# Kernel tuning notes

Hardware: AMD Instinct MI355X
Metric: run time of the kernel (lower is better)

Reference implementation:

```python
import jax, jax.numpy as jnp
import numpy as np

N = 117000   # vocab / number of WordNet synsets (square adjacency)
E = 500000   # number of COO edges
B, T = 4, 64 # batch, seq len


def setup_inputs() -> dict:
    key = jax.random.key(0)
    k1, k2, k3, k4 = jax.random.split(key, 4)
    logits = jax.random.normal(k1, (B, T, N), dtype=jnp.float32)
    # ensure every row index appears at least once so row-normalization never divides by zero
    row = jnp.concatenate([jnp.arange(N, dtype=jnp.int32),
                           jax.random.randint(k2, (E - N,), 0, N, dtype=jnp.int32)])
    col = jax.random.randint(k3, (E,), 0, N, dtype=jnp.int32)
    edge_index = jnp.stack([row, col], axis=0)  # [2, E]
    vv = jax.random.uniform(k4, (E,), dtype=jnp.float32, minval=0.1, maxval=1.0)
    return {"logits": logits, "vv": vv, "edge_index": edge_index}


def reference(logits, vv, edge_index):
    # StructuredLogits.forward with DEHARDCODE_ALPHA=1.0, renormalize=True:
    #   neighbors = spmm(A, logits_flat^T)^T ; neighbors /= row_sum ; out = neighbors + logits
    row, col = edge_index[0], edge_index[1]
    n = logits.shape[-1]
    x = logits.reshape(-1, n).T                              # [N, BT]
    contrib = vv[:, None] * x[col]                           # [E, BT] gather + scale
    neigh_T = jax.ops.segment_sum(contrib, row, num_segments=n)   # [N, BT] scatter-add (SpMM)
    row_sum = jax.ops.segment_sum(vv, row, num_segments=n)        # [N] row-normalizer
    neighbors = (neigh_T / row_sum[:, None]).T.reshape(logits.shape)
    return neighbors + logits
```

## Files before the change

kernel.cpp:

```cpp
#include <hip/hip_runtime.h>
#include <hip/hip_fp16.h>

#define NN 117000
#define BT 256

#define SCAN_CHUNK 1024
#define SCAN_NB ((NN + SCAN_CHUNK - 1) / SCAN_CHUNK)
#define SCAN_P2_T 128

#define ROWS_PB 32
#define LDS_STRIDE (BT + 2)

union U8 { uint2 u; __half2 h[2]; };


__global__ void hist_kernel(const int* __restrict__ row, int* __restrict__ count, int E) {
    int e = blockIdx.x * blockDim.x + threadIdx.x;
    if (e < E) atomicAdd(&count[row[e]], 1);
}

__global__ void scan_phase1(const int* __restrict__ count, int* __restrict__ block_sums) {
    __shared__ int s[256];
    int base = blockIdx.x * SCAN_CHUNK + threadIdx.x * 4;
    int sum = 0;
#pragma unroll
    for (int j = 0; j < 4; ++j) {
        int idx = base + j;
        if (idx < NN) sum += count[idx];
    }
    s[threadIdx.x] = sum;
    __syncthreads();
    for (int off = 128; off > 0; off >>= 1) {
        if (threadIdx.x < off) s[threadIdx.x] += s[threadIdx.x + off];
        __syncthreads();
    }
    if (threadIdx.x == 0) block_sums[blockIdx.x] = s[0];
}

__global__ void scan_phase2(int* __restrict__ block_sums, int* __restrict__ row_ptr) {
    __shared__ int s[SCAN_P2_T];
    int t = threadIdx.x;
    int v = (t < SCAN_NB) ? block_sums[t] : 0;
    s[t] = v;
    __syncthreads();
    for (int off = 1; off < SCAN_P2_T; off <<= 1) {
        int u = (t >= off) ? s[t - off] : 0;
        __syncthreads();
        s[t] += u;
        __syncthreads();
    }
    if (t < SCAN_NB) block_sums[t] = (t == 0) ? 0 : s[t - 1];
    if (t == SCAN_P2_T - 1) row_ptr[NN] = s[SCAN_NB - 1];
}

__global__ void scan_phase3(int* __restrict__ row_ptr, const int* __restrict__ block_offs,
                            int* __restrict__ cursor) {
    __shared__ int s[256];
    int base = blockIdx.x * SCAN_CHUNK + threadIdx.x * 4;
    int v[4];
    int sum = 0;
#pragma unroll
    for (int j = 0; j < 4; ++j) {
        int idx = base + j;
        v[j] = (idx < NN) ? row_ptr[idx] : 0;
        sum += v[j];
    }
    s[threadIdx.x] = sum;
    __syncthreads();
    for (int off = 1; off < 256; off <<= 1) {
        int u = (threadIdx.x >= off) ? s[threadIdx.x - off] : 0;
        __syncthreads();
        s[threadIdx.x] += u;
        __syncthreads();
    }
    int prefix = block_offs[blockIdx.x] + ((threadIdx.x == 0) ? 0 : s[threadIdx.x - 1]);
#pragma unroll
    for (int j = 0; j < 4; ++j) {
        int idx = base + j;
        if (idx < NN) {
            row_ptr[idx] = prefix;
            cursor[idx]  = prefix;
            prefix += v[j];
        }
    }
}

__global__ void scatter_kernel(const int* __restrict__ row, const int* __restrict__ col,
                               const float* __restrict__ vv, int* __restrict__ cursor,
                               int2* __restrict__ edge_s, int E) {
    int e = blockIdx.x * blockDim.x + threadIdx.x;
    if (e >= E) return;
    int p = atomicAdd(&cursor[row[e]], 1);
    edge_s[p] = make_int2(col[e], __float_as_int(vv[e]));
}


__global__ void transpose_h_kernel(const float* __restrict__ logits, __half* __restrict__ xT) {
    __shared__ float s[64][33];
    int tx = threadIdx.x & 31;
    int ty = threadIdx.x >> 5;
    int i0  = blockIdx.x * 32;
    int bt0 = blockIdx.y * 64;
    int i = i0 + tx;
    if (i < NN) {
#pragma unroll
        for (int r = 0; r < 8; ++r) {
            int bt = bt0 + ty + r * 8;
            s[ty + r * 8][tx] = logits[(size_t)bt * NN + i];
        }
    }
    __syncthreads();
#pragma unroll
    for (int r = 0; r < 4; ++r) {
        int il = ty + r * 8;
        int i2 = i0 + il;
        if (i2 < NN) {
            __half2 h = __floats2half2_rn(s[2 * tx][il], s[2 * tx + 1][il]);
            ((__half2*)(xT + (size_t)i2 * BT + bt0))[tx] = h;
        }
    }
}

__global__ void row_gather_fused_kernel(const int* __restrict__ row_ptr,
                                        const int2* __restrict__ edge_s,
                                        const __half* __restrict__ xT,
                                        const float* __restrict__ logits,
                                        float* __restrict__ out) {
    __shared__ float s[ROWS_PB][LDS_STRIDE];
    int wave = threadIdx.x >> 6;
    int lane = threadIdx.x & 63;
    int i0 = blockIdx.x * ROWS_PB;
    const uint2* xT2 = (const uint2*)xT;

#pragma unroll
    for (int rr = 0; rr < 4; ++rr) {
        int r_local = wave * 4 + rr;
        int i = i0 + r_local;
        if (i < NN) {
            int k0 = row_ptr[i], k1 = row_ptr[i + 1];
            float4 acc = make_float4(0.f, 0.f, 0.f, 0.f);
            float rs = 0.f;
            for (int kb = k0; kb < k1; kb += 64) {
                int nk = min(64, k1 - kb);
                int2 ed = make_int2(0, 0);
                if (lane < nk) ed = edge_s[kb + lane];
                int   ccol = ed.x;
                float cval = __int_as_float(ed.y);
                int c0 = __shfl(ccol, 0);
                uint2 cur = xT2[(size_t)c0 * (BT / 4) + lane];
                for (int j = 0; j < nk; ++j) {
                    uint2 nxt = make_uint2(0u, 0u);
                    if (j + 1 < nk) {
                        int cn = __shfl(ccol, j + 1);
                        nxt = xT2[(size_t)cn * (BT / 4) + lane];
                    }
                    float v = __shfl(cval, j);
                    rs += v;
                    U8 t; t.u = cur;
                    float2 fa = __half22float2(t.h[0]);
                    float2 fb = __half22float2(t.h[1]);
                    acc.x += v * fa.x; acc.y += v * fa.y;
                    acc.z += v * fb.x; acc.w += v * fb.y;
                    cur = nxt;
                }
            }
            float inv = (rs > 0.f) ? (1.0f / rs) : 0.f;
            float2* sp = (float2*)&s[r_local][lane * 4];
            sp[0] = make_float2(acc.x * inv, acc.y * inv);
            sp[1] = make_float2(acc.z * inv, acc.w * inv);
        }
    }
    __syncthreads();

    int tx = threadIdx.x & 31;
    int ty = threadIdx.x >> 5;
    int i = i0 + tx;
    if (i < NN) {
#pragma unroll
        for (int r = 0; r < 16; ++r) {
            int bt = r * 16 + ty;
            size_t idx = (size_t)bt * NN + i;
            out[idx] = logits[idx] + s[tx][bt];
        }
    }
}


__global__ void transpose_kernel(const float* __restrict__ logits, float* __restrict__ xT) {
    __shared__ float s[32][33];
    int tx = threadIdx.x & 31;
    int ty = threadIdx.x >> 5;
    int i0  = blockIdx.x * 32;
    int bt0 = blockIdx.y * 32;
    int i = i0 + tx;
#pragma unroll
    for (int r = 0; r < 4; ++r) {
        int bt = bt0 + ty + r * 8;
        if (i < NN) s[ty + r * 8][tx] = logits[(size_t)bt * NN + i];
    }
    __syncthreads();
#pragma unroll
    for (int r = 0; r < 4; ++r) {
        int i2 = i0 + ty + r * 8;
        if (i2 < NN) xT[(size_t)i2 * BT + bt0 + tx] = s[tx][ty + r * 8];
    }
}

__global__ void rowsum_kernel(const int* __restrict__ row, const float* __restrict__ vv,
                              float* __restrict__ row_sum, int E) {
    int e = blockIdx.x * blockDim.x + threadIdx.x;
    if (e < E) atomicAdd(&row_sum[row[e]], vv[e]);
}

__global__ void edge_kernel(const int* __restrict__ row, const int* __restrict__ col,
                            const float* __restrict__ vv, const float* __restrict__ xT,
                            float* __restrict__ acc, int E) {
    int e = blockIdx.x * 4 + (threadIdx.x >> 6);
    if (e >= E) return;
    int lane = threadIdx.x & 63;
    int r = row[e];
    int c = col[e];
    float v = vv[e];
    float4 x4 = ((const float4*)(xT + (size_t)c * BT))[lane];
    float* dst = acc + (size_t)r * BT + lane * 4;
    atomicAdd(dst + 0, v * x4.x);
    atomicAdd(dst + 1, v * x4.y);
    atomicAdd(dst + 2, v * x4.z);
    atomicAdd(dst + 3, v * x4.w);
}

__global__ void finalize_div_kernel(const float* __restrict__ logits, const float* __restrict__ acc,
                                    const float* __restrict__ row_sum, float* __restrict__ out) {
    __shared__ float s[32][33];
    __shared__ float rs[32];
    int tx = threadIdx.x & 31;
    int ty = threadIdx.x >> 5;
    int i0  = blockIdx.x * 32;
    int bt0 = blockIdx.y * 32;
#pragma unroll
    for (int r = 0; r < 4; ++r) {
        int il = ty + r * 8;
        int i = i0 + il;
        if (i < NN) s[il][tx] = acc[(size_t)i * BT + bt0 + tx];
    }
    if (threadIdx.x < 32) {
        int i = i0 + (int)threadIdx.x;
        rs[threadIdx.x] = (i < NN) ? row_sum[i] : 1.0f;
    }
    __syncthreads();
#pragma unroll
    for (int r = 0; r < 4; ++r) {
        int bt = bt0 + ty + r * 8;
        int i = i0 + tx;
        if (i < NN) {
            size_t idx = (size_t)bt * NN + i;
            out[idx] = logits[idx] + s[tx][ty + r * 8] / rs[tx];
        }
    }
}

extern "C" void kernel_launch(void* const* d_in, const int* in_sizes, int n_in,
                              void* d_out, int out_size, void* d_ws, size_t ws_size,
                              hipStream_t stream) {
    const float* logits = (const float*)d_in[0];
    const float* vv     = (const float*)d_in[1];
    const int*   ei     = (const int*)d_in[2];
    const int E = in_sizes[1];
    const int* row = ei;
    const int* col = ei + E;
    float* out = (float*)d_out;

    const size_t accN = (size_t)NN * BT;

    const int e_blocks = (E + 255) / 256;

    const size_t need_csr = (size_t)E * sizeof(int2)
                          + accN * sizeof(__half)
                          + (size_t)(NN + 1 + NN + SCAN_NB) * sizeof(int);

    if (ws_size >= need_csr) {
        int2*   edge_s     = (int2*)d_ws;
        __half* xT         = (__half*)(edge_s + E);
        int*    row_ptr    = (int*)(xT + accN);
        int*    cursor     = row_ptr + (NN + 1);
        int*    block_sums = cursor + NN;

        dim3 tgrid((NN + 31) / 32, BT / 64);
        const int fuse_blocks = (NN + ROWS_PB - 1) / ROWS_PB;

        hipMemsetAsync(row_ptr, 0, (NN + 1) * sizeof(int), stream);
        hist_kernel<<<e_blocks, 256, 0, stream>>>(row, row_ptr, E);
        scan_phase1<<<SCAN_NB, 256, 0, stream>>>(row_ptr, block_sums);
        scan_phase2<<<1, SCAN_P2_T, 0, stream>>>(block_sums, row_ptr);
        scan_phase3<<<SCAN_NB, 256, 0, stream>>>(row_ptr, block_sums, cursor);
        scatter_kernel<<<e_blocks, 256, 0, stream>>>(row, col, vv, cursor, edge_s, E);
        transpose_h_kernel<<<tgrid, 256, 0, stream>>>(logits, xT);
        row_gather_fused_kernel<<<fuse_blocks, 512, 0, stream>>>(row_ptr, edge_s, xT,
                                                                 logits, out);
    } else {
        float* acc     = (float*)d_ws;
        float* xT      = acc + accN;
        float* row_sum = xT + accN;
        dim3 tgrid32((NN + 31) / 32, BT / 32);
        hipMemsetAsync(acc, 0, accN * sizeof(float), stream);
        hipMemsetAsync(row_sum, 0, NN * sizeof(float), stream);
        rowsum_kernel<<<e_blocks, 256, 0, stream>>>(row, vv, row_sum, E);
        transpose_kernel<<<tgrid32, 256, 0, stream>>>(logits, xT);
        edge_kernel<<<(E + 3) / 4, 256, 0, stream>>>(row, col, vv, xT, acc, E);
        finalize_div_kernel<<<tgrid32, 256, 0, stream>>>(logits, acc, row_sum, out);
    }
}
```

Before: 377.8 us.

## Process each wave's four rows as one merged edge stream with deeper gather prefetch

```diff
diff --git a/kernel.cpp b/kernel.cpp
--- a/kernel.cpp
+++ b/kernel.cpp
@@ -9,7 +9,7 @@
 #define SCAN_P2_T 128
 
 #define ROWS_PB 32
-#define LDS_STRIDE (BT + 2)
+#define LDS_STRIDE 257
 
 union U8 { uint2 u; __half2 h[2]; };
 
@@ -130,45 +130,86 @@
     int wave = threadIdx.x >> 6;
     int lane = threadIdx.x & 63;
     int i0 = blockIdx.x * ROWS_PB;
+    int iw = i0 + wave * 4;
     const uint2* xT2 = (const uint2*)xT;
 
-#pragma unroll
-    for (int rr = 0; rr < 4; ++rr) {
-        int r_local = wave * 4 + rr;
-        int i = i0 + r_local;
-        if (i < NN) {
-            int k0 = row_ptr[i], k1 = row_ptr[i + 1];
-            float4 acc = make_float4(0.f, 0.f, 0.f, 0.f);
-            float rs = 0.f;
-            for (int kb = k0; kb < k1; kb += 64) {
-                int nk = min(64, k1 - kb);
-                int2 ed = make_int2(0, 0);
-                if (lane < nk) ed = edge_s[kb + lane];
-                int   ccol = ed.x;
-                float cval = __int_as_float(ed.y);
-                int c0 = __shfl(ccol, 0);
-                uint2 cur = xT2[(size_t)c0 * (BT / 4) + lane];
-                for (int j = 0; j < nk; ++j) {
-                    uint2 nxt = make_uint2(0u, 0u);
-                    if (j + 1 < nk) {
-                        int cn = __shfl(ccol, j + 1);
-                        nxt = xT2[(size_t)cn * (BT / 4) + lane];
-                    }
-                    float v = __shfl(cval, j);
-                    rs += v;
-                    U8 t; t.u = cur;
-                    float2 fa = __half22float2(t.h[0]);
-                    float2 fb = __half22float2(t.h[1]);
-                    acc.x += v * fa.x; acc.y += v * fa.y;
-                    acc.z += v * fb.x; acc.w += v * fb.y;
-                    cur = nxt;
-                }
+    if (iw < NN) {
+        int rp = 0;
+        if (lane < 5) {
+            int idx = iw + lane;
+            if (idx > NN) idx = NN;
+            rp = row_ptr[idx];
+        }
+        int kw0 = __shfl(rp, 0);
+        int b0  = __shfl(rp, 1);
+        int b1  = __shfl(rp, 2);
+        int b2  = __shfl(rp, 3);
+        int b3  = __shfl(rp, 4);
+        int kw1 = b3;
+
+        float4 acc = make_float4(0.f, 0.f, 0.f, 0.f);
+        float rs = 0.f;
+        int r_cur = 0;
+        int next_b = b0;
+
+#define FINALIZE_ROW() do {                                                   \
+            float inv = (rs > 0.f) ? (1.0f / rs) : 0.f;                       \
+            int rl = (wave << 2) + r_cur;                                     \
+            s[rl][0 * 64 + lane] = acc.x * inv;                               \
+            s[rl][1 * 64 + lane] = acc.y * inv;                               \
+            s[rl][2 * 64 + lane] = acc.z * inv;                               \
+            s[rl][3 * 64 + lane] = acc.w * inv;                               \
+            acc = make_float4(0.f, 0.f, 0.f, 0.f);                            \
+            rs = 0.f;                                                         \
+            ++r_cur;                                                          \
+            next_b = (r_cur == 1) ? b1 : ((r_cur == 2) ? b2 : b3);            \
+        } while (0)
+
+        while (r_cur < 4 && next_b == kw0) FINALIZE_ROW();
+
+        for (int kb = kw0; kb < kw1; kb += 64) {
+            int nk = min(64, kw1 - kb);
+            int2 ed = make_int2(0, 0);
+            if (lane < nk) ed = edge_s[kb + lane];
+            int   ccol = ed.x;
+            float cval = __int_as_float(ed.y);
+
+            uint2 p0 = make_uint2(0u, 0u), p1 = p0, p2 = p0, p3 = p0;
+#define ISSUE(dst, jj) do {                                                   \
+                if ((jj) < nk) {                                              \
+                    int cn = __shfl(ccol, (jj));                              \
+                    dst = xT2[(size_t)cn * (BT / 4) + lane];                  \
+                }                                                             \
+            } while (0)
+            ISSUE(p0, 0); ISSUE(p1, 1); ISSUE(p2, 2); ISSUE(p3, 3);
+
+#define CONSUME(pp, jj) do {                                                  \
+                if ((jj) < nk) {                                              \
+                    float v = __shfl(cval, (jj));                             \
+                    rs += v;                                                  \
+                    U8 t; t.u = pp;                                           \
+                    float2 fa = __half22float2(t.h[0]);                       \
+                    float2 fb = __half22float2(t.h[1]);                       \
+                    acc.x += v * fa.x; acc.y += v * fa.y;                     \
+                    acc.z += v * fb.x; acc.w += v * fb.y;                     \
+                    int kg = kb + (jj) + 1;                                   \
+                    while (r_cur < 4 && kg == next_b) FINALIZE_ROW();         \
+                }                                                             \
+            } while (0)
+
+            for (int j = 0; j < nk; j += 4) {
+                uint2 q0 = make_uint2(0u, 0u), q1 = q0, q2 = q0, q3 = q0;
+                ISSUE(q0, j + 4); ISSUE(q1, j + 5); ISSUE(q2, j + 6); ISSUE(q3, j + 7);
+                CONSUME(p0, j + 0);
+                CONSUME(p1, j + 1);
+                CONSUME(p2, j + 2);
+                CONSUME(p3, j + 3);
+                p0 = q0; p1 = q1; p2 = q2; p3 = q3;
             }
-            float inv = (rs > 0.f) ? (1.0f / rs) : 0.f;
-            float2* sp = (float2*)&s[r_local][lane * 4];
-            sp[0] = make_float2(acc.x * inv, acc.y * inv);
-            sp[1] = make_float2(acc.z * inv, acc.w * inv);
-        }
+#undef ISSUE
+#undef CONSUME
+        }
+#undef FINALIZE_ROW
     }
     __syncthreads();
 
@@ -179,8 +220,9 @@
 #pragma unroll
         for (int r = 0; r < 16; ++r) {
             int bt = r * 16 + ty;
+            int c = ((bt & 3) << 6) + (bt >> 2);
             size_t idx = (size_t)bt * NN + i;
-            out[idx] = logits[idx] + s[tx][bt];
+            out[idx] = logits[idx] + s[tx][c];
         }
     }
 }
```

Result: faster. 367.8 us (-2.6%).
